# Kernel tuning notes

Measured on AMD Instinct MI355X. Metric: run time of the kernel, lower is better.

The kernel has to match this reference:

```python
import jax, jax.numpy as jnp
import numpy as np

B, S, H = 16, 128, 768
L, K = 2, 4
NORM_ITEM = 0.5


def _xavier(key, shape):
    fan_in, fan_out = shape[-1], shape[-2]
    std = float(np.sqrt(2.0 / (fan_in + fan_out)))
    return jax.random.normal(key, shape, dtype=jnp.float32) * std


def setup_inputs() -> dict:
    key = jax.random.key(0)
    ks = jax.random.split(key, 13)
    sentences = jax.random.normal(ks[0], (B, S, H), dtype=jnp.float32)
    adj_matrix = jax.random.uniform(ks[1], (B, K, S, S), dtype=jnp.float32)
    return {
        "sentences": sentences,
        "adj_matrix": adj_matrix,
        # stacked per-(layer, dep_kind) parameters
        "W_in": _xavier(ks[2], (L, K, H, H)),
        "b_in": _xavier(ks[3], (L, K, H, 1)),
        "W_out": _xavier(ks[4], (L, K, H, H)),
        "b_out": _xavier(ks[5], (L, K, H, 1)),
        "Wg_in": _xavier(ks[6], (L, K, H, H)),
        "bg_in": _xavier(ks[7], (L, K, H, 1)),
        "Wg_out": _xavier(ks[8], (L, K, H, H)),
        "bg_out": _xavier(ks[9], (L, K, H, 1)),
        "W_loop": _xavier(ks[10], (L, H, H)),
    }


def reference(sentences, adj_matrix, W_in, b_in, W_out, b_out,
              Wg_in, bg_in, Wg_out, bg_out, W_loop):
    # sentences: [B,S,H], adj_matrix: [B,K,S,S]
    adj_in = adj_matrix                       # message along edges
    adj_out = jnp.swapaxes(adj_matrix, 2, 3)  # reversed edges
    h = jnp.swapaxes(sentences, 1, 2)         # [B,H,S]

    def conv(Wg, bg, W, b, adj, h):
        # Wg,W: [K,H,H]; bg,b: [K,H,1]; adj: [B,K,S,S]; h: [B,H,S]
        gate = jax.nn.sigmoid(jnp.einsum('khd,bds->bkhs', Wg, h) + bg[None])
        rel = NORM_ITEM * gate * (jnp.einsum('khd,bds->bkhs', W, h) + b[None])
        # bmm with adjacency, then sum over dep kinds
        return jnp.einsum('bkhs,bkst->bht', rel, adj)

    n_layers = W_in.shape[0]
    for l in range(n_layers):
        s = jnp.einsum('hd,bds->bhs', W_loop[l], h)  # self loop
        s = s + conv(Wg_in[l], bg_in[l], W_in[l], b_in[l], adj_in, h)
        s = s + conv(Wg_out[l], bg_out[l], W_out[l], b_out[l], adj_out, h)
        h = jax.nn.relu(s)
    return jnp.swapaxes(h, 1, 2)  # [B,S,H]
```

## Files before the change

kernel.cpp:

```cpp
#include <hip/hip_runtime.h>
#include <stdint.h>

#define B_ 16
#define S_ 128
#define H_ 768
#define K_ 4
#define L_ 2
#define T_ (B_*S_)

typedef __attribute__((ext_vector_type(4))) float f32x4;
typedef __attribute__((ext_vector_type(8))) short s16x8;
typedef __bf16 bf16x8 __attribute__((ext_vector_type(8)));
typedef unsigned short u16;

__device__ inline u16 f2bf(float f) {
    union { float f; uint32_t u; } v; v.f = f;
    uint32_t u = v.u;
    return (u16)((u + 0x7fffu + ((u >> 16) & 1u)) >> 16);
}

__device__ inline ushort4 f2bf4(float4 v) {
    ushort4 r; r.x = f2bf(v.x); r.y = f2bf(v.y); r.z = f2bf(v.z); r.w = f2bf(v.w);
    return r;
}

template <typename T>
__device__ inline auto mfma_impl(T a, T b, f32x4 c, int)
    -> decltype(__builtin_amdgcn_mfma_f32_16x16x32_bf16(a, b, c, 0, 0, 0)) {
    return __builtin_amdgcn_mfma_f32_16x16x32_bf16(a, b, c, 0, 0, 0);
}
template <typename T>
__device__ inline f32x4 mfma_impl(T a, T b, f32x4 c, long) {
    return __builtin_amdgcn_mfma_f32_16x16x32_bf16(
        __builtin_bit_cast(bf16x8, a), __builtin_bit_cast(bf16x8, b), c, 0, 0, 0);
}
__device__ inline f32x4 mfma16(s16x8 a, s16x8 b, f32x4 c) {
    return mfma_impl(a, b, c, 0);
}

__device__ inline void gload_lds16(const void* g, void* l) {
    __builtin_amdgcn_global_load_lds(
        (__attribute__((address_space(1))) void*)(g),
        (__attribute__((address_space(3))) void*)(l), 16, 0, 0);
}

__device__ inline void stage_tile(const char* gbase, int rowStrideBytes, u16* lds, int tid) {
    const int lane = tid & 63;
    const int w = tid >> 6;
    const int lr = lane >> 3;
    const int cb = (lane & 7) << 4;
    #pragma unroll
    for (int j = 0; j < 4; ++j) {
        const int seg = j * 4 + w;
        const int row = seg * 8 + lr;
        const int sb = cb ^ ((row & 7) << 4);
        gload_lds16(gbase + (size_t)row * rowStrideBytes + sb,
                    lds + seg * 512);
    }
}

__device__ inline void stage64(const char* gbase, int rowStrideBytes, char* lds, int tid) {
    const int lane = tid & 63;
    const int w = tid >> 6;
    const int lr = lane >> 3;
    const int cb = (lane & 7) << 4;
    #pragma unroll
    for (int j = 0; j < 2; ++j) {
        const int seg = j * 4 + w;
        const int row = seg * 8 + lr;
        const int sb = cb ^ ((row & 7) << 4);
        gload_lds16(gbase + (size_t)row * rowStrideBytes + sb,
                    lds + seg * 1024);
    }
}

__device__ inline void stage32x128(const char* g, int strideB, char* lds, int tid) {
    const int lane = tid & 63;
    const int w = tid >> 6;
    #pragma unroll
    for (int j = 0; j < 2; ++j) {
        const int r = j * 64 + w * 16 + (lane >> 2);
        gload_lds16(g + (size_t)r * strideB + ((lane & 3) << 4),
                    lds + j * 4096 + w * 1024);
    }
}

__device__ inline s16x8 read_frag(const u16* lds, int row, int colByte) {
    const int bir = colByte ^ ((row & 7) << 4);
    return *(const s16x8*)((const char*)lds + row * 128 + bir);
}

__device__ inline s16x8 rf32(const u16* lds, int row, int cb) {
    return *(const s16x8*)((const char*)lds + row * 64 + cb);
}

__global__ void prep_weights(const float* __restrict__ Wg_in, const float* __restrict__ Wg_out,
                             const float* __restrict__ W_in,  const float* __restrict__ W_out,
                             const float* __restrict__ W_loop, const float* __restrict__ sent,
                             u16* __restrict__ Wg_all, u16* __restrict__ W_all,
                             u16* __restrict__ Wl, u16* __restrict__ X0) {
    const int i4 = blockIdx.x * blockDim.x + threadIdx.x;
    const int NW4 = L_ * K_ * H_ * H_ / 4;
    const int KHH4 = K_ * H_ * H_ / 4;
    if (i4 < NW4) {
        const int l = i4 / KHH4;
        const int rem = i4 - l * KHH4;
        const int d0 = (l * 2) * KHH4 + rem;
        const int d1 = d0 + KHH4;
        ((ushort4*)Wg_all)[d0] = f2bf4(((const float4*)Wg_in)[i4]);
        ((ushort4*)Wg_all)[d1] = f2bf4(((const float4*)Wg_out)[i4]);
        ((ushort4*)W_all)[d0]  = f2bf4(((const float4*)W_in)[i4]);
        ((ushort4*)W_all)[d1]  = f2bf4(((const float4*)W_out)[i4]);
    }
    if (i4 < L_ * H_ * H_ / 4)  ((ushort4*)Wl)[i4] = f2bf4(((const float4*)W_loop)[i4]);
    if (i4 < T_ * H_ / 4)       ((ushort4*)X0)[i4] = f2bf4(((const float4*)sent)[i4]);
}

__global__ void prep_adj(const float* __restrict__ adj, u16* __restrict__ adjA) {
    const int idx = blockIdx.x * blockDim.x + threadIdx.x;
    const int s = idx & 127;
    const int t = (idx >> 7) & 127;
    const int b = (idx >> 14) & 15;
    const int p = idx >> 18;
    const int dir = p >> 2, k = p & 3;
    const float v = dir ? adj[(((size_t)b * K_ + k) * S_ + t) * S_ + s]
                        : adj[(((size_t)b * K_ + k) * S_ + s) * S_ + t];
    adjA[idx] = f2bf(v);
}

__global__ __launch_bounds__(256, 2)
void gemm1_kernel(const u16* __restrict__ Xb,
                  const u16* __restrict__ Wg_all, const u16* __restrict__ W_all,
                  const u16* __restrict__ Wl,
                  const float* __restrict__ bg_in, const float* __restrict__ bg_out,
                  const float* __restrict__ b_in,  const float* __restrict__ b_out,
                  int layer,
                  u16* __restrict__ Rel2, float* __restrict__ SBuf) {
    __shared__ __align__(16) char smem[49152];

    const int tid = threadIdx.x;
    const int lane = tid & 63;
    const int w = tid >> 6;
    const int wm = w >> 1;
    const int wn = w & 1;
    const int l15 = lane & 15;
    const int hi16 = (lane >> 4) << 4;
    const int p = blockIdx.z;
    const bool gated = (p < 8);
    if (!gated && blockIdx.y >= 3) return;
    const int m0 = blockIdx.x * 128;
    const int n0 = gated ? blockIdx.y * 128 : blockIdx.y * 256;

    const u16* Wr;
    const u16* Wg = nullptr;
    if (gated) {
        const int dir = p >> 2, k = p & 3;
        const size_t woff = ((size_t)(layer * 2 + dir) * K_ + k) * (size_t)(H_ * H_);
        Wg = Wg_all + woff;
        Wr = W_all + woff;
    } else {
        Wr = Wl + (size_t)layer * H_ * H_;
    }

    const char* gA  = (const char*)Xb + (size_t)m0 * (H_ * 2);
    const char* gBr = (const char*)Wr + (size_t)n0 * (H_ * 2);
    const char* gBg = gated ? ((const char*)Wg + (size_t)n0 * (H_ * 2))
                            : (gBr + (size_t)128 * (H_ * 2));

    auto STAGE = [&](int kt, int c) {
        char* base = smem + c * 24576;
        const size_t kb = (size_t)kt * 64;
        stage32x128(gA  + kb, H_ * 2, base,         tid);
        stage32x128(gBr + kb, H_ * 2, base + 8192,  tid);
        stage32x128(gBg + kb, H_ * 2, base + 16384, tid);
    };

    const f32x4 zf = {0.f, 0.f, 0.f, 0.f};
    f32x4 accr[4][4], accg[4][4];
    #pragma unroll
    for (int i = 0; i < 4; ++i)
        #pragma unroll
        for (int j = 0; j < 4; ++j) { accr[i][j] = zf; accg[i][j] = zf; }

    STAGE(0, 0);
    __syncthreads();

    for (int t = 0; t < 24; ++t) {
        const int c = t & 1;
        if (t < 23) STAGE(t + 1, c ^ 1);
        const u16* lA  = (const u16*)(smem + c * 24576);
        const u16* lBr = (const u16*)(smem + c * 24576 + 8192);
        const u16* lBg = (const u16*)(smem + c * 24576 + 16384);
        s16x8 a[4], br[4], bg[4];
        #pragma unroll
        for (int i = 0; i < 4; ++i)
            a[i] = rf32(lA, wm * 64 + i * 16 + l15, hi16);
        #pragma unroll
        for (int j = 0; j < 4; ++j)
            br[j] = rf32(lBr, wn * 64 + j * 16 + l15, hi16);
        #pragma unroll
        for (int j = 0; j < 4; ++j)
            bg[j] = rf32(lBg, wn * 64 + j * 16 + l15, hi16);
        #pragma unroll
        for (int i = 0; i < 4; ++i) {
            #pragma unroll
            for (int j = 0; j < 4; ++j) {
                accr[i][j] = mfma16(a[i], br[j], accr[i][j]);
                accg[i][j] = mfma16(a[i], bg[j], accg[i][j]);
            }
        }
        __syncthreads();
    }

    if (gated) {
        const int dir = p >> 2, k = p & 3;
        const float* bgp = (dir ? bg_out : bg_in) + ((size_t)layer * K_ + k) * H_;
        const float* brp = (dir ? b_out  : b_in ) + ((size_t)layer * K_ + k) * H_;
        const int b = blockIdx.x;
        #pragma unroll
        for (int j = 0; j < 4; ++j) {
            const int h = n0 + wn * 64 + j * 16 + l15;
            const float bgv = bgp[h];
            const float brv = brp[h];
            #pragma unroll
            for (int i = 0; i < 4; ++i) {
                const int s0 = wm * 64 + i * 16 + ((lane >> 4) << 2);
                u16 tmp[4];
                #pragma unroll
                for (int r = 0; r < 4; ++r) {
                    const float g = accg[i][j][r] + bgv;
                    const float v = accr[i][j][r] + brv;
                    tmp[r] = f2bf(0.5f * v / (1.f + __expf(-g)));
                }
                ushort4 pk; pk.x = tmp[0]; pk.y = tmp[1]; pk.z = tmp[2]; pk.w = tmp[3];
                *(ushort4*)(Rel2 + (((size_t)p * B_ + b) * H_ + h) * S_ + s0) = pk;
            }
        }
    } else {
        #pragma unroll
        for (int j = 0; j < 4; ++j) {
            const int h1 = n0 + wn * 64 + j * 16 + l15;
            const int h2 = h1 + 128;
            #pragma unroll
            for (int i = 0; i < 4; ++i) {
                const int tg = m0 + wm * 64 + i * 16 + ((lane >> 4) << 2);
                #pragma unroll
                for (int r = 0; r < 4; ++r) {
                    SBuf[(size_t)(tg + r) * H_ + h1] = accr[i][j][r];
                    SBuf[(size_t)(tg + r) * H_ + h2] = accg[i][j][r];
                }
            }
        }
    }
}

__global__ __launch_bounds__(256, 2)
void gemm2_kernel(const u16* __restrict__ adjA, const u16* __restrict__ Rel2,
                  const float* __restrict__ SBuf,
                  u16* __restrict__ Xn, float* __restrict__ Out, int lastLayer) {
    __shared__ __align__(16) char smem2[49152];

    const int tid = threadIdx.x;
    const int lane = tid & 63;
    const int w = tid >> 6;
    const int wm = w >> 1, wn = w & 1;
    const int l15 = lane & 15;
    const int hi16 = (lane >> 4) << 4;
    const int h0 = blockIdx.x * 64;
    const int b = blockIdx.y;

    auto STAGE = [&](int q, int c) {
        const int p = q >> 1, sc = q & 1;
        const char* Ab = (const char*)adjA + ((size_t)p * B_ + b) * (S_ * S_ * 2) + sc * 128;
        const char* Bb = (const char*)Rel2 + (((size_t)p * B_ + b) * H_ + h0) * (S_ * 2) + sc * 128;
        char* base = smem2 + c * 24576;
        stage_tile(Ab, S_ * 2, (u16*)base, tid);
        stage64(Bb, S_ * 2, base + 16384, tid);
    };

    const f32x4 zf = {0.f, 0.f, 0.f, 0.f};
    f32x4 acc[4][2];
    #pragma unroll
    for (int i = 0; i < 4; ++i)
        #pragma unroll
        for (int j = 0; j < 2; ++j) acc[i][j] = zf;

    STAGE(0, 0);
    __syncthreads();

    for (int q = 0; q < 16; ++q) {
        const int c = q & 1;
        if (q < 15) STAGE(q + 1, c ^ 1);
        const u16* lA = (const u16*)(smem2 + c * 24576);
        const u16* lB = (const u16*)(smem2 + c * 24576 + 16384);
        #pragma unroll
        for (int kq = 0; kq < 2; ++kq) {
            const int ck = kq * 64 + hi16;
            s16x8 a[4], bb[2];
            #pragma unroll
            for (int i = 0; i < 4; ++i)
                a[i] = read_frag(lA, wm * 64 + i * 16 + l15, ck);
            #pragma unroll
            for (int j = 0; j < 2; ++j)
                bb[j] = read_frag(lB, wn * 32 + j * 16 + l15, ck);
            #pragma unroll
            for (int i = 0; i < 4; ++i)
                #pragma unroll
                for (int j = 0; j < 2; ++j)
                    acc[i][j] = mfma16(a[i], bb[j], acc[i][j]);
        }
        __syncthreads();
    }

    #pragma unroll
    for (int i = 0; i < 4; ++i) {
        const int tl = wm * 64 + i * 16 + ((lane >> 4) << 2);
        #pragma unroll
        for (int j = 0; j < 2; ++j) {
            const int h = h0 + wn * 32 + j * 16 + l15;
            #pragma unroll
            for (int r = 0; r < 4; ++r) {
                const size_t t = (size_t)b * S_ + tl + r;
                float v = acc[i][j][r] + SBuf[t * H_ + h];
                v = fmaxf(v, 0.f);
                if (lastLayer) Out[t * H_ + h] = v;
                else           Xn[t * H_ + h] = f2bf(v);
            }
        }
    }
}

extern "C" void kernel_launch(void* const* d_in, const int* in_sizes, int n_in,
                              void* d_out, int out_size, void* d_ws, size_t ws_size,
                              hipStream_t stream) {
    const float* sent   = (const float*)d_in[0];
    const float* adj    = (const float*)d_in[1];
    const float* W_in   = (const float*)d_in[2];
    const float* b_in   = (const float*)d_in[3];
    const float* W_out  = (const float*)d_in[4];
    const float* b_out  = (const float*)d_in[5];
    const float* Wg_in  = (const float*)d_in[6];
    const float* bg_in  = (const float*)d_in[7];
    const float* Wg_out = (const float*)d_in[8];
    const float* bg_out = (const float*)d_in[9];
    const float* W_loop = (const float*)d_in[10];

    char* ws = (char*)d_ws;
    u16* Wg_all = (u16*)(ws);
    u16* W_all  = (u16*)(ws + 18874368);
    u16* Wl     = (u16*)(ws + 37748736);
    u16* adjA   = (u16*)(ws + 40108032);
    u16* X0     = (u16*)(ws + 44302336);
    u16* X1     = (u16*)(ws + 47448064);
    u16* Rel2   = (u16*)(ws + 50593792);
    float* SBuf = (float*)(ws + 75759616);

    prep_weights<<<4608, 256, 0, stream>>>(Wg_in, Wg_out, W_in, W_out, W_loop, sent,
                                           Wg_all, W_all, Wl, X0);
    prep_adj<<<8192, 256, 0, stream>>>(adj, adjA);

    u16* Xc = X0;
    u16* Xn = X1;
    for (int l = 0; l < L_; ++l) {
        gemm1_kernel<<<dim3(16, 6, 9), 256, 0, stream>>>(Xc, Wg_all, W_all, Wl,
                                                         bg_in, bg_out, b_in, b_out,
                                                         l, Rel2, SBuf);
        gemm2_kernel<<<dim3(12, 16), 256, 0, stream>>>(adjA, Rel2, SBuf, Xn,
                                                       (float*)d_out, l == L_ - 1);
        u16* t = Xc; Xc = Xn; Xn = t;
    }
}
```

Baseline: 179.1 us.

## Prepack weights into MFMA fragment layout and load B operands directly to registers

Weights are repacked into an MFMA-fragment-ordered bf16 layout, so gemm1 reads its B operands straight from global memory into registers with register double-buffering, and only the activation tile goes through LDS, now with a swizzled layout. The grid becomes a flat 1D launch of exactly the needed blocks, remapped so consecutive blocks spread across weight matrices, and the MFMA section runs at raised wave priority. This aims to cut LDS traffic and footprint, drop early-exit idle blocks and overlap loads with compute. In exchange, the weight-packing kernel uses a shared-memory transpose stage, and the direct global B loads depend on L2 hit rates.

Measured after the change: 186.6 us. 1.04x slower.

```diff
diff --git a/kernel.cpp b/kernel.cpp
--- a/kernel.cpp
+++ b/kernel.cpp
@@ -54,8 +54,7 @@
         const int seg = j * 4 + w;
         const int row = seg * 8 + lr;
         const int sb = cb ^ ((row & 7) << 4);
-        gload_lds16(gbase + (size_t)row * rowStrideBytes + sb,
-                    lds + seg * 512);
+        gload_lds16(gbase + (size_t)row * rowStrideBytes + sb, lds + seg * 512);
     }
 }
 
@@ -69,19 +68,7 @@
         const int seg = j * 4 + w;
         const int row = seg * 8 + lr;
         const int sb = cb ^ ((row & 7) << 4);
-        gload_lds16(gbase + (size_t)row * rowStrideBytes + sb,
-                    lds + seg * 1024);
-    }
-}
-
-__device__ inline void stage32x128(const char* g, int strideB, char* lds, int tid) {
-    const int lane = tid & 63;
-    const int w = tid >> 6;
-    #pragma unroll
-    for (int j = 0; j < 2; ++j) {
-        const int r = j * 64 + w * 16 + (lane >> 2);
-        gload_lds16(g + (size_t)r * strideB + ((lane & 3) << 4),
-                    lds + j * 4096 + w * 1024);
+        gload_lds16(gbase + (size_t)row * rowStrideBytes + sb, lds + seg * 1024);
     }
 }
 
@@ -90,30 +77,14 @@
     return *(const s16x8*)((const char*)lds + row * 128 + bir);
 }
 
-__device__ inline s16x8 rf32(const u16* lds, int row, int cb) {
-    return *(const s16x8*)((const char*)lds + row * 64 + cb);
-}
-
-__global__ void prep_weights(const float* __restrict__ Wg_in, const float* __restrict__ Wg_out,
-                             const float* __restrict__ W_in,  const float* __restrict__ W_out,
-                             const float* __restrict__ W_loop, const float* __restrict__ sent,
-                             u16* __restrict__ Wg_all, u16* __restrict__ W_all,
-                             u16* __restrict__ Wl, u16* __restrict__ X0) {
+__device__ inline s16x8 rf32s(const u16* lds, int row, int cb) {
+    const int bir = cb ^ (((row >> 1) & 3) << 4);
+    return *(const s16x8*)((const char*)lds + row * 64 + bir);
+}
+
+__global__ void prep_x(const float* __restrict__ sent, u16* __restrict__ X0) {
     const int i4 = blockIdx.x * blockDim.x + threadIdx.x;
-    const int NW4 = L_ * K_ * H_ * H_ / 4;
-    const int KHH4 = K_ * H_ * H_ / 4;
-    if (i4 < NW4) {
-        const int l = i4 / KHH4;
-        const int rem = i4 - l * KHH4;
-        const int d0 = (l * 2) * KHH4 + rem;
-        const int d1 = d0 + KHH4;
-        ((ushort4*)Wg_all)[d0] = f2bf4(((const float4*)Wg_in)[i4]);
-        ((ushort4*)Wg_all)[d1] = f2bf4(((const float4*)Wg_out)[i4]);
-        ((ushort4*)W_all)[d0]  = f2bf4(((const float4*)W_in)[i4]);
-        ((ushort4*)W_all)[d1]  = f2bf4(((const float4*)W_out)[i4]);
-    }
-    if (i4 < L_ * H_ * H_ / 4)  ((ushort4*)Wl)[i4] = f2bf4(((const float4*)W_loop)[i4]);
-    if (i4 < T_ * H_ / 4)       ((ushort4*)X0)[i4] = f2bf4(((const float4*)sent)[i4]);
+    if (i4 < T_ * H_ / 4) ((ushort4*)X0)[i4] = f2bf4(((const float4*)sent)[i4]);
 }
 
 __global__ void prep_adj(const float* __restrict__ adj, u16* __restrict__ adjA) {
@@ -128,15 +99,55 @@
     adjA[idx] = f2bf(v);
 }
 
+__global__ void pack_weights(const float* __restrict__ W_in,  const float* __restrict__ W_out,
+                             const float* __restrict__ Wg_in, const float* __restrict__ Wg_out,
+                             const float* __restrict__ W_loop, u16* __restrict__ Wpk) {
+    __shared__ float slab[16][772];
+    const int tid = threadIdx.x;
+    const int bid = blockIdx.x;
+    const int nT  = bid % 48;
+    const int mat = (bid / 48) % 17;
+    const int l   = bid / (48 * 17);
+
+    const float* src;
+    if (mat < 16) {
+        const int p = mat >> 1, slot = mat & 1;
+        const int dir = p >> 2, k = p & 3;
+        const float* t = slot ? (dir ? Wg_out : Wg_in) : (dir ? W_out : W_in);
+        src = t + ((size_t)l * K_ + k) * (H_ * H_);
+    } else {
+        src = W_loop + (size_t)l * (H_ * H_);
+    }
+    #pragma unroll
+    for (int it = 0; it < 12; ++it) {
+        const int idx = it * 256 + tid;
+        const int row = idx / 192, c4 = idx % 192;
+        *(float4*)&slab[row][c4 * 4] = ((const float4*)(src + (size_t)(nT * 16 + row) * H_))[c4];
+    }
+    __syncthreads();
+    const int q = tid >> 6, lane = tid & 63;
+    const int n = lane & 15, ks = lane >> 4;
+    u16* outBase = Wpk + ((((size_t)l * 17 + mat) * 48 + nT) * 24) * 512;
+    #pragma unroll
+    for (int it = 0; it < 6; ++it) {
+        const int kT = it * 4 + q;
+        u16 tmp[8];
+        #pragma unroll
+        for (int u = 0; u < 8; ++u) tmp[u] = f2bf(slab[n][kT * 32 + ks * 8 + u]);
+        s16x8 v;
+        #pragma unroll
+        for (int u = 0; u < 8; ++u) v[u] = (short)tmp[u];
+        *(s16x8*)(outBase + (size_t)kT * 512 + lane * 8) = v;
+    }
+}
+
 __global__ __launch_bounds__(256, 2)
-void gemm1_kernel(const u16* __restrict__ Xb,
-                  const u16* __restrict__ Wg_all, const u16* __restrict__ W_all,
-                  const u16* __restrict__ Wl,
+void gemm1_kernel(const u16* __restrict__ Xb, const u16* __restrict__ Wpk,
                   const float* __restrict__ bg_in, const float* __restrict__ bg_out,
                   const float* __restrict__ b_in,  const float* __restrict__ b_out,
                   int layer,
                   u16* __restrict__ Rel2, float* __restrict__ SBuf) {
-    __shared__ __align__(16) char smem[49152];
+    __shared__ __align__(16) char smem[16384];
 
     const int tid = threadIdx.x;
     const int lane = tid & 63;
@@ -145,34 +156,40 @@
     const int wn = w & 1;
     const int l15 = lane & 15;
     const int hi16 = (lane >> 4) << 4;
-    const int p = blockIdx.z;
-    const bool gated = (p < 8);
-    if (!gated && blockIdx.y >= 3) return;
-    const int m0 = blockIdx.x * 128;
-    const int n0 = gated ? blockIdx.y * 128 : blockIdx.y * 256;
-
-    const u16* Wr;
-    const u16* Wg = nullptr;
-    if (gated) {
-        const int dir = p >> 2, k = p & 3;
-        const size_t woff = ((size_t)(layer * 2 + dir) * K_ + k) * (size_t)(H_ * H_);
-        Wg = Wg_all + woff;
-        Wr = W_all + woff;
-    } else {
-        Wr = Wl + (size_t)layer * H_ * H_;
-    }
-
-    const char* gA  = (const char*)Xb + (size_t)m0 * (H_ * 2);
-    const char* gBr = (const char*)Wr + (size_t)n0 * (H_ * 2);
-    const char* gBg = gated ? ((const char*)Wg + (size_t)n0 * (H_ * 2))
-                            : (gBr + (size_t)128 * (H_ * 2));
-
-    auto STAGE = [&](int kt, int c) {
-        char* base = smem + c * 24576;
-        const size_t kb = (size_t)kt * 64;
-        stage32x128(gA  + kb, H_ * 2, base,         tid);
-        stage32x128(gBr + kb, H_ * 2, base + 8192,  tid);
-        stage32x128(gBg + kb, H_ * 2, base + 16384, tid);
+
+    const int id = blockIdx.x;
+    const int id2 = (id & 7) * 102 + (id >> 3);
+    int p, y, m;
+    if (id2 < 768) { p = id2 / 96; const int r = id2 % 96; y = r / 16; m = r % 16; }
+    else           { const int q = id2 - 768; p = 8; y = q / 16; m = q % 16; }
+    const int m0 = m * 128;
+
+    const u16* pkL = Wpk + (size_t)layer * 17 * 589824;
+    const int matR = (p < 8) ? p * 2     : 16;
+    const int matG = (p < 8) ? p * 2 + 1 : 16;
+    const int nbr  = (p < 8) ? y * 8     : y * 16;
+    const int nbg  = (p < 8) ? y * 8     : y * 16 + 8;
+    const u16* pR = pkL + ((size_t)matR * 48 + nbr + wn * 4) * (24 * 512) + lane * 8;
+    const u16* pG = pkL + ((size_t)matG * 48 + nbg + wn * 4) * (24 * 512) + lane * 8;
+    const char* gA = (const char*)Xb + (size_t)m0 * (H_ * 2);
+
+    auto STAGE_A = [&](int kt, int c) {
+        char* base = smem + c * 8192;
+        #pragma unroll
+        for (int j = 0; j < 2; ++j) {
+            const int rr = (j * 4 + w) * 16 + (lane >> 2);
+            const int cbl = (lane & 3) << 4;
+            const int sc = cbl ^ (((rr >> 1) & 3) << 4);
+            gload_lds16(gA + (size_t)rr * (H_ * 2) + kt * 64 + sc,
+                        base + (j * 4 + w) * 1024);
+        }
+    };
+    auto LOADB = [&](s16x8* dst, int kt) {
+        #pragma unroll
+        for (int j = 0; j < 4; ++j) {
+            dst[j]     = *(const s16x8*)(pR + ((size_t)j * 24 + kt) * 512);
+            dst[4 + j] = *(const s16x8*)(pG + ((size_t)j * 24 + kt) * 512);
+        }
     };
 
     const f32x4 zf = {0.f, 0.f, 0.f, 0.f};
@@ -182,44 +199,49 @@
         #pragma unroll
         for (int j = 0; j < 4; ++j) { accr[i][j] = zf; accg[i][j] = zf; }
 
-    STAGE(0, 0);
-    __syncthreads();
-
-    for (int t = 0; t < 24; ++t) {
-        const int c = t & 1;
-        if (t < 23) STAGE(t + 1, c ^ 1);
-        const u16* lA  = (const u16*)(smem + c * 24576);
-        const u16* lBr = (const u16*)(smem + c * 24576 + 8192);
-        const u16* lBg = (const u16*)(smem + c * 24576 + 16384);
-        s16x8 a[4], br[4], bg[4];
+    s16x8 bA[8], bB[8];
+
+    STAGE_A(0, 0);
+    __builtin_amdgcn_sched_barrier(0);
+    LOADB(bA, 0);
+
+    auto body = [&](int t, s16x8* cur, s16x8* nxt, bool pf) {
+        asm volatile("s_waitcnt vmcnt(8)" ::: "memory");
+        __builtin_amdgcn_s_barrier();
+        const u16* lA = (const u16*)(smem + (t & 1) * 8192);
+        s16x8 a[4];
         #pragma unroll
         for (int i = 0; i < 4; ++i)
-            a[i] = rf32(lA, wm * 64 + i * 16 + l15, hi16);
-        #pragma unroll
-        for (int j = 0; j < 4; ++j)
-            br[j] = rf32(lBr, wn * 64 + j * 16 + l15, hi16);
-        #pragma unroll
-        for (int j = 0; j < 4; ++j)
-            bg[j] = rf32(lBg, wn * 64 + j * 16 + l15, hi16);
+            a[i] = rf32s(lA, wm * 64 + i * 16 + l15, hi16);
+        if (pf) {
+            STAGE_A(t + 1, (t + 1) & 1);
+            __builtin_amdgcn_sched_barrier(0);
+            LOADB(nxt, t + 1);
+        }
+        __builtin_amdgcn_s_setprio(1);
         #pragma unroll
         for (int i = 0; i < 4; ++i) {
             #pragma unroll
             for (int j = 0; j < 4; ++j) {
-                accr[i][j] = mfma16(a[i], br[j], accr[i][j]);
-                accg[i][j] = mfma16(a[i], bg[j], accg[i][j]);
+                accr[i][j] = mfma16(a[i], cur[j],     accr[i][j]);
+                accg[i][j] = mfma16(a[i], cur[4 + j], accg[i][j]);
             }
         }
-        __syncthreads();
-    }
-
-    if (gated) {
+        __builtin_amdgcn_s_setprio(0);
+    };
+
+    for (int t = 0; t < 24; t += 2) {
+        body(t,     bA, bB, true);
+        body(t + 1, bB, bA, t + 1 < 23);
+    }
+
+    if (p < 8) {
         const int dir = p >> 2, k = p & 3;
         const float* bgp = (dir ? bg_out : bg_in) + ((size_t)layer * K_ + k) * H_;
         const float* brp = (dir ? b_out  : b_in ) + ((size_t)layer * K_ + k) * H_;
-        const int b = blockIdx.x;
         #pragma unroll
         for (int j = 0; j < 4; ++j) {
-            const int h = n0 + wn * 64 + j * 16 + l15;
+            const int h = y * 128 + wn * 64 + j * 16 + l15;
             const float bgv = bgp[h];
             const float brv = brp[h];
             #pragma unroll
@@ -233,13 +255,13 @@
                     tmp[r] = f2bf(0.5f * v / (1.f + __expf(-g)));
                 }
                 ushort4 pk; pk.x = tmp[0]; pk.y = tmp[1]; pk.z = tmp[2]; pk.w = tmp[3];
-                *(ushort4*)(Rel2 + (((size_t)p * B_ + b) * H_ + h) * S_ + s0) = pk;
+                *(ushort4*)(Rel2 + (((size_t)p * B_ + m) * H_ + h) * S_ + s0) = pk;
             }
         }
     } else {
         #pragma unroll
         for (int j = 0; j < 4; ++j) {
-            const int h1 = n0 + wn * 64 + j * 16 + l15;
+            const int h1 = y * 256 + wn * 64 + j * 16 + l15;
             const int h2 = h1 + 128;
             #pragma unroll
             for (int i = 0; i < 4; ++i) {
@@ -346,25 +368,22 @@
     const float* W_loop = (const float*)d_in[10];
 
     char* ws = (char*)d_ws;
-    u16* Wg_all = (u16*)(ws);
-    u16* W_all  = (u16*)(ws + 18874368);
-    u16* Wl     = (u16*)(ws + 37748736);
+    u16* Wpk    = (u16*)(ws);
     u16* adjA   = (u16*)(ws + 40108032);
     u16* X0     = (u16*)(ws + 44302336);
     u16* X1     = (u16*)(ws + 47448064);
     u16* Rel2   = (u16*)(ws + 50593792);
     float* SBuf = (float*)(ws + 75759616);
 
-    prep_weights<<<4608, 256, 0, stream>>>(Wg_in, Wg_out, W_in, W_out, W_loop, sent,
-                                           Wg_all, W_all, Wl, X0);
+    prep_x<<<1536, 256, 0, stream>>>(sent, X0);
     prep_adj<<<8192, 256, 0, stream>>>(adj, adjA);
+    pack_weights<<<L_ * 17 * 48, 256, 0, stream>>>(W_in, W_out, Wg_in, Wg_out, W_loop, Wpk);
 
     u16* Xc = X0;
     u16* Xn = X1;
     for (int l = 0; l < L_; ++l) {
-        gemm1_kernel<<<dim3(16, 6, 9), 256, 0, stream>>>(Xc, Wg_all, W_all, Wl,
-                                                         bg_in, bg_out, b_in, b_out,
-                                                         l, Rel2, SBuf);
+        gemm1_kernel<<<816, 256, 0, stream>>>(Xc, Wpk, bg_in, bg_out, b_in, b_out,
+                                              l, Rel2, SBuf);
         gemm2_kernel<<<dim3(12, 16), 256, 0, stream>>>(adjA, Rel2, SBuf, Xn,
                                                        (float*)d_out, l == L_ - 1);
         u16* t = Xc; Xc = Xn; Xn = t;
```
